# Optimization experiments

Hardware: AMD Instinct MI355X
Metric: run time of the kernel (lower is better)

## Reference

```python
import jax, jax.numpy as jnp
import numpy as np

D_MODEL = 1024
N_HEADS = 16
FF_DIM = 4096
EPS = 1e-05


def setup_inputs() -> dict:
    key = jax.random.key(0)
    ks = jax.random.split(key, 8)
    B, T, E, F = 4, 2048, D_MODEL, FF_DIM
    s = 0.02
    return {
        "encoder_input": jax.random.normal(ks[0], (B, T, E), jnp.float32),
        "source_padding_masks": jax.random.randint(ks[1], (B, T), 0, 2, jnp.int32),
        "Wq": jax.random.normal(ks[2], (E, E), jnp.float32) * s,
        "Wk": jax.random.normal(ks[3], (E, E), jnp.float32) * s,
        "Wv": jax.random.normal(ks[4], (E, E), jnp.float32) * s,
        "Wo": jax.random.normal(ks[5], (E, E), jnp.float32) * s,
        "w1": jax.random.normal(ks[6], (F, E), jnp.float32) * s,
        "b1": jnp.zeros((F,), jnp.float32),
        "w2": jax.random.normal(ks[7], (E, F), jnp.float32) * s,
        "b2": jnp.zeros((E,), jnp.float32),
        "ln_g": jnp.ones((E,), jnp.float32),
        "ln_b": jnp.zeros((E,), jnp.float32),
    }


def _layer_norm(x, g, b):
    # Faithful to the custom LayerNorm: unbiased std (ddof=1), eps added to sd.
    mean = jnp.mean(x, axis=-1, keepdims=True)
    sd = jnp.std(x, axis=-1, keepdims=True, ddof=1)
    return (x - mean) / (sd + EPS) * g + b


def reference(encoder_input, source_padding_masks, Wq, Wk, Wv, Wo, w1, b1, w2, b2, ln_g, ln_b):
    x = encoder_input
    B, T, E = x.shape
    H, hd = N_HEADS, E // N_HEADS

    q = (x @ Wq.T).reshape(B, T, H, hd).transpose(0, 2, 1, 3)  # [B,H,T,hd]
    k = (x @ Wk.T).reshape(B, T, H, hd).transpose(0, 2, 1, 3)
    v = (x @ Wv.T).reshape(B, T, H, hd).transpose(0, 2, 1, 3)

    scores = jnp.einsum("bhqd,bhkd->bhqk", q, k) / jnp.sqrt(jnp.float32(hd))
    key_mask = source_padding_masks[:, None, None, :]  # [B,1,1,T]
    scores = jnp.where(key_mask == 0, -jnp.inf, scores)
    attn = jax.nn.softmax(scores, axis=-1)
    attn = attn * source_padding_masks[:, None, :, None].astype(attn.dtype)  # query mask post-softmax

    ctx = jnp.einsum("bhqk,bhkd->bhqd", attn, v)
    ctx = ctx.transpose(0, 2, 1, 3).reshape(B, T, E)
    att_out = ctx @ Wo.T

    # residual block 1 (dropout is identity in eval)
    h = _layer_norm(att_out + x, ln_g, ln_b)

    ff = jax.nn.relu(h @ w1.T + b1) @ w2.T + b2
    # residual block 2 (same shared LayerNorm params)
    out = _layer_norm(ff + h, ln_g, ln_b)
    return out
```

## Files before the change

### kernel.cpp

```cpp
#include <hip/hip_runtime.h>
#include <hip/hip_bf16.h>


typedef __attribute__((ext_vector_type(8))) short  short8;
typedef __attribute__((ext_vector_type(4))) float  f32x4;
typedef __attribute__((ext_vector_type(4))) int    i32x4;
typedef __attribute__((ext_vector_type(4))) unsigned short u16x4;

__device__ inline float b2f(unsigned short u) {
    unsigned int x = ((unsigned int)u) << 16;
    return __builtin_bit_cast(float, x);
}
__device__ inline unsigned short f2b(float f) {
    return __builtin_bit_cast(unsigned short, __float2bfloat16(f));
}

__device__ inline void llds16(const unsigned short* g, unsigned short* l) {
    __builtin_amdgcn_global_load_lds(
        (const __attribute__((address_space(1))) unsigned int*)g,
        (__attribute__((address_space(3))) unsigned int*)l, 16, 0, 0);
}

__device__ inline int swz(int row, int col8) {
    return (row << 6) + (((col8 ^ (row >> 1)) & 7) << 3);
}

__global__ __launch_bounds__(256)
void cast_f32_bf16(const float* __restrict__ in, unsigned short* __restrict__ out,
                   int n4)
{
    int i = blockIdx.x * 256 + threadIdx.x;
    if (i >= n4) return;
    f32x4 v = *(const f32x4*)(in + (size_t)i * 4);
    u16x4 o;
    for (int j = 0; j < 4; ++j) o[j] = f2b(v[j]);
    *(u16x4*)(out + (size_t)i * 4) = o;
}

__global__ __launch_bounds__(256)
void mask_bf16(const int* __restrict__ m, unsigned short* __restrict__ mb, int n)
{
    int i = blockIdx.x * 256 + threadIdx.x;
    if (i < n) mb[i] = m[i] ? (unsigned short)0x3F80 : (unsigned short)0;
}

template <int BIAS, int RELU, int VT>
__global__ __launch_bounds__(256, 2)
void gemm_bt(const unsigned short* __restrict__ A,
             const unsigned short* __restrict__ W,
             const float* __restrict__ bias,
             const int* __restrict__ mask,
             unsigned short* __restrict__ C,
             int M, int N, int K)
{
    __shared__ __attribute__((aligned(16))) unsigned short a_s[128 * 64];
    __shared__ __attribute__((aligned(16))) unsigned short b_s[128 * 64];

    const int tid  = threadIdx.x;
    const int lane = tid & 63;
    const int w    = tid >> 6;
    const int ln   = lane & 15;
    const int quad = lane >> 4;
    const int wm   = w >> 1, wn = w & 1;
    const int bm   = blockIdx.y, bn = blockIdx.x;

    f32x4 acc[4][4] = {};

    const int nkt = K >> 6;
    for (int kt = 0; kt < nkt; ++kt) {
        for (int i = 0; i < 4; ++i) {
            int e   = i * 256 + tid;
            int row = e >> 3;
            int c8  = (e & 7) ^ ((e >> 4) & 7);
            llds16(A + (size_t)(bm * 128 + row) * K + kt * 64 + c8 * 8, &a_s[e * 8]);
            llds16(W + (size_t)(bn * 128 + row) * K + kt * 64 + c8 * 8, &b_s[e * 8]);
        }
        __syncthreads();
        for (int ks = 0; ks < 2; ++ks) {
            short8 af[4], bf_[4];
            for (int mt = 0; mt < 4; ++mt)
                af[mt] = *(const short8*)&a_s[swz(wm * 64 + mt * 16 + ln, ks * 4 + quad)];
            for (int nt = 0; nt < 4; ++nt)
                bf_[nt] = *(const short8*)&b_s[swz(wn * 64 + nt * 16 + ln, ks * 4 + quad)];
            for (int mt = 0; mt < 4; ++mt)
                for (int nt = 0; nt < 4; ++nt)
                    acc[mt][nt] = __builtin_amdgcn_mfma_f32_16x16x32_bf16(
                        af[mt], bf_[nt], acc[mt][nt], 0, 0, 0);
        }
        __syncthreads();
    }

    if (VT) {
        const int T2 = 2048, H2 = 16;
        for (int mt = 0; mt < 4; ++mt) {
            int row0 = bm * 128 + wm * 64 + mt * 16 + quad * 4;
            int bb = row0 >> 11, t0 = row0 & 2047;
            i32x4 mi = *(const i32x4*)&mask[bb * 2048 + t0];
            for (int nt = 0; nt < 4; ++nt) {
                int col = bn * 128 + wn * 64 + nt * 16 + ln;
                int hh2 = col >> 6, d = col & 63;
                u16x4 o;
                for (int r = 0; r < 4; ++r)
                    o[r] = mi[r] ? f2b(acc[mt][nt][r]) : (unsigned short)0;
                *(u16x4*)(C + ((size_t)((bb * H2 + hh2) * 64 + d)) * T2 + t0) = o;
            }
        }
    } else {
        for (int nt = 0; nt < 4; ++nt) {
            int col = bn * 128 + wn * 64 + nt * 16 + ln;
            float bv = 0.f;
            if (BIAS) bv = bias[col];
            for (int mt = 0; mt < 4; ++mt) {
                int row0 = bm * 128 + wm * 64 + mt * 16 + quad * 4;
                for (int r = 0; r < 4; ++r) {
                    float v = acc[mt][nt][r] + bv;
                    if (RELU) v = v > 0.f ? v : 0.f;
                    C[(size_t)(row0 + r) * N + col] = f2b(v);
                }
            }
        }
    }
}

__global__ __launch_bounds__(256, 4)
void flash_attn3(const unsigned short* __restrict__ Q,
                 const unsigned short* __restrict__ K,
                 const unsigned short* __restrict__ Vt,
                 const unsigned short* __restrict__ mb,
                 const int* __restrict__ mask,
                 unsigned short* __restrict__ O,
                 int T, int H, int E)
{
    __shared__ __attribute__((aligned(16))) unsigned short k_s[2][64 * 64];
    __shared__ __attribute__((aligned(16))) unsigned short v_s[2][64 * 64];
    __shared__ __attribute__((aligned(16))) unsigned short p_s[64 * 64];

    const int qt = blockIdx.x, h = blockIdx.y, b = blockIdx.z;
    const int tid  = threadIdx.x;
    const int w    = tid >> 6;
    const int lane = tid & 63;
    const int ln   = lane & 15;
    const int quad = lane >> 4;
    const int q0   = qt * 64;
    const unsigned short* vt_b = Vt + (size_t)(b * H + h) * 64 * T;

    for (int i = 0; i < 2; ++i) {
        int e = i * 256 + tid;
        int row = e >> 3;
        int c8  = (e & 7) ^ ((e >> 4) & 7);
        llds16(Q + (size_t)(b * T + q0 + row) * E + h * 64 + c8 * 8, &p_s[e * 8]);
        llds16(K + (size_t)(b * T + row) * E + h * 64 + c8 * 8, &k_s[0][e * 8]);
        llds16(vt_b + (size_t)row * T + c8 * 8, &v_s[0][e * 8]);
    }
    __syncthreads();
    short8 aq[2];
    aq[0] = *(const short8*)&p_s[w * 1024 + swz(ln, quad)];
    aq[1] = *(const short8*)&p_s[w * 1024 + swz(ln, 4 + quad)];

    f32x4 Oa[4] = {};
    f32x4 lacc = {};
    const float SCL = 0.125f * 1.44269504f;

    const int nkb = T >> 6;
    for (int kb = 0; kb < nkb; ++kb) {
        const int cur = kb & 1;
        if (kb + 1 < nkb) {
            for (int i = 0; i < 2; ++i) {
                int e = i * 256 + tid;
                int row = e >> 3;
                int c8  = (e & 7) ^ ((e >> 4) & 7);
                llds16(K + (size_t)(b * T + (kb + 1) * 64 + row) * E + h * 64 + c8 * 8,
                       &k_s[cur ^ 1][e * 8]);
                llds16(vt_b + (size_t)row * T + (kb + 1) * 64 + c8 * 8,
                       &v_s[cur ^ 1][e * 8]);
            }
        }
        short8 mf0 = *(const short8*)&mb[b * T + kb * 64 + quad * 8];
        short8 mf1 = *(const short8*)&mb[b * T + kb * 64 + 32 + quad * 8];

        f32x4 S[4] = {};
        for (int ks = 0; ks < 2; ++ks)
            for (int nt = 0; nt < 4; ++nt) {
                short8 bf_ = *(const short8*)&k_s[cur][swz(nt * 16 + ln, ks * 4 + quad)];
                S[nt] = __builtin_amdgcn_mfma_f32_16x16x32_bf16(aq[ks], bf_, S[nt], 0, 0, 0);
            }
        for (int nt = 0; nt < 4; ++nt)
            for (int r = 0; r < 4; ++r) {
                float p = exp2f(S[nt][r] * SCL);
                p_s[w * 1024 + swz(quad * 4 + r, 2 * nt + (ln >> 3)) + (ln & 7)] = f2b(p);
            }
        short8 ap0 = *(const short8*)&p_s[w * 1024 + swz(ln, quad)];
        short8 ap1 = *(const short8*)&p_s[w * 1024 + swz(ln, 4 + quad)];
        lacc = __builtin_amdgcn_mfma_f32_16x16x32_bf16(ap0, mf0, lacc, 0, 0, 0);
        lacc = __builtin_amdgcn_mfma_f32_16x16x32_bf16(ap1, mf1, lacc, 0, 0, 0);
        for (int nt = 0; nt < 4; ++nt) {
            short8 bv0 = *(const short8*)&v_s[cur][swz(nt * 16 + ln, quad)];
            Oa[nt] = __builtin_amdgcn_mfma_f32_16x16x32_bf16(ap0, bv0, Oa[nt], 0, 0, 0);
            short8 bv1 = *(const short8*)&v_s[cur][swz(nt * 16 + ln, 4 + quad)];
            Oa[nt] = __builtin_amdgcn_mfma_f32_16x16x32_bf16(ap1, bv1, Oa[nt], 0, 0, 0);
        }
        __syncthreads();
    }

    for (int r = 0; r < 4; ++r) {
        int qrow = q0 + w * 16 + quad * 4 + r;
        float inv = mask[b * T + qrow] ? 1.f / lacc[r] : 0.f;
        for (int nt = 0; nt < 4; ++nt)
            O[(size_t)(b * T + qrow) * E + h * 64 + nt * 16 + ln] = f2b(Oa[nt][r] * inv);
    }
}

template <int R_F32, int O_F32>
__global__ __launch_bounds__(256, 4)
void ln_residual(const unsigned short* __restrict__ A,
                 const void* __restrict__ R,
                 const float* __restrict__ G,
                 const float* __restrict__ Bt,
                 void* __restrict__ Y, int E)
{
    const int row = blockIdx.x;
    const int tid = threadIdx.x;
    size_t base = (size_t)row * E + tid * 4;
    u16x4 a4 = *(const u16x4*)(A + base);
    float rv[4];
    if (R_F32) {
        f32x4 r4 = *(const f32x4*)((const float*)R + base);
        for (int j = 0; j < 4; ++j) rv[j] = r4[j];
    } else {
        u16x4 r4 = *(const u16x4*)((const unsigned short*)R + base);
        for (int j = 0; j < 4; ++j) rv[j] = b2f(r4[j]);
    }
    float v[4]; float s = 0.f, sq = 0.f;
    for (int j = 0; j < 4; ++j) {
        v[j] = b2f(a4[j]) + rv[j];
        s += v[j]; sq += v[j] * v[j];
    }
    for (int o = 32; o; o >>= 1) {
        s  += __shfl_xor(s, o, 64);
        sq += __shfl_xor(sq, o, 64);
    }
    __shared__ float red[8];
    int w = tid >> 6, lane = tid & 63;
    if (lane == 0) { red[w] = s; red[4 + w] = sq; }
    __syncthreads();
    s  = red[0] + red[1] + red[2] + red[3];
    sq = red[4] + red[5] + red[6] + red[7];
    float mean = s / E;
    float var  = (sq - s * mean) / (E - 1);
    var = fmaxf(var, 0.f);
    float inv = 1.f / (sqrtf(var) + 1e-5f);
    f32x4 g4 = *(const f32x4*)(G + tid * 4);
    f32x4 b4 = *(const f32x4*)(Bt + tid * 4);
    if (O_F32) {
        f32x4 o4;
        for (int j = 0; j < 4; ++j)
            o4[j] = (v[j] - mean) * inv * g4[j] + b4[j];
        *(f32x4*)((float*)Y + base) = o4;
    } else {
        u16x4 o4;
        for (int j = 0; j < 4; ++j)
            o4[j] = f2b((v[j] - mean) * inv * g4[j] + b4[j]);
        *(u16x4*)((unsigned short*)Y + base) = o4;
    }
}

extern "C" void kernel_launch(void* const* d_in, const int* in_sizes, int n_in,
                              void* d_out, int out_size, void* d_ws, size_t ws_size,
                              hipStream_t stream)
{
    const int B = 4, T = 2048, E = 1024, F = 4096, H = 16;
    const int M = B * T;

    const float* x  = (const float*)d_in[0];
    const int* mask = (const int*)d_in[1];
    const float* Wq = (const float*)d_in[2];
    const float* Wk = (const float*)d_in[3];
    const float* Wv = (const float*)d_in[4];
    const float* Wo = (const float*)d_in[5];
    const float* w1 = (const float*)d_in[6];
    const float* b1 = (const float*)d_in[7];
    const float* w2 = (const float*)d_in[8];
    const float* b2 = (const float*)d_in[9];
    const float* lg = (const float*)d_in[10];
    const float* lb = (const float*)d_in[11];
    float* out = (float*)d_out;

    char* ws = (char*)d_ws;
    const size_t MB = 1024 * 1024;
    unsigned short* xb  = (unsigned short*)(ws);
    unsigned short* q   = (unsigned short*)(ws + 16 * MB);
    unsigned short* kk  = (unsigned short*)(ws + 32 * MB);
    unsigned short* vt  = (unsigned short*)(ws + 48 * MB);
    unsigned short* ctx = (unsigned short*)(ws + 64 * MB);
    unsigned short* hh  = (unsigned short*)(ws + 80 * MB);
    unsigned short* mbf = hh;
    unsigned short* ff1 = (unsigned short*)(ws);
    unsigned short* ff2 = ctx;
    unsigned short* att = q;
    unsigned short* Wqb = (unsigned short*)(ws + 96 * MB);
    unsigned short* Wkb = (unsigned short*)(ws + 98 * MB);
    unsigned short* Wvb = (unsigned short*)(ws + 100 * MB);
    unsigned short* Wob = (unsigned short*)(ws + 102 * MB);
    unsigned short* w1b = (unsigned short*)(ws + 104 * MB);
    unsigned short* w2b = (unsigned short*)(ws + 112 * MB);

    dim3 blk(256);
    cast_f32_bf16<<<dim3(M * E / 4 / 256), blk, 0, stream>>>(x,  xb,  M * E / 4);
    cast_f32_bf16<<<dim3(E * E / 4 / 256), blk, 0, stream>>>(Wq, Wqb, E * E / 4);
    cast_f32_bf16<<<dim3(E * E / 4 / 256), blk, 0, stream>>>(Wk, Wkb, E * E / 4);
    cast_f32_bf16<<<dim3(E * E / 4 / 256), blk, 0, stream>>>(Wv, Wvb, E * E / 4);
    cast_f32_bf16<<<dim3(E * E / 4 / 256), blk, 0, stream>>>(Wo, Wob, E * E / 4);
    cast_f32_bf16<<<dim3(F * E / 4 / 256), blk, 0, stream>>>(w1, w1b, F * E / 4);
    cast_f32_bf16<<<dim3(F * E / 4 / 256), blk, 0, stream>>>(w2, w2b, F * E / 4);
    mask_bf16<<<dim3(M / 256), blk, 0, stream>>>(mask, mbf, M);

    gemm_bt<0, 0, 0><<<dim3(E / 128, M / 128), blk, 0, stream>>>(xb, Wqb, nullptr, nullptr, q,  M, E, E);
    gemm_bt<0, 0, 0><<<dim3(E / 128, M / 128), blk, 0, stream>>>(xb, Wkb, nullptr, nullptr, kk, M, E, E);
    gemm_bt<0, 0, 1><<<dim3(E / 128, M / 128), blk, 0, stream>>>(xb, Wvb, nullptr, mask, vt, M, E, E);
    flash_attn3<<<dim3(T / 64, H, B), blk, 0, stream>>>(q, kk, vt, mbf, mask, ctx, T, H, E);
    gemm_bt<0, 0, 0><<<dim3(E / 128, M / 128), blk, 0, stream>>>(ctx, Wob, nullptr, nullptr, att, M, E, E);
    ln_residual<1, 0><<<dim3(M), blk, 0, stream>>>(att, x, lg, lb, hh, E);
    gemm_bt<1, 1, 0><<<dim3(F / 128, M / 128), blk, 0, stream>>>(hh, w1b, b1, nullptr, ff1, M, F, E);
    gemm_bt<1, 0, 0><<<dim3(E / 128, M / 128), blk, 0, stream>>>(ff1, w2b, b2, nullptr, ff2, M, E, F);
    ln_residual<0, 1><<<dim3(M), blk, 0, stream>>>(ff2, hh, lg, lb, out, E);
}
```

Before: 585.3 us.

## Rewrite flash attention with 32x32 MFMA, register-resident P, and prescaled Q

```diff
diff --git a/kernel.cpp b/kernel.cpp
--- a/kernel.cpp
+++ b/kernel.cpp
@@ -2,10 +2,12 @@
 #include <hip/hip_bf16.h>
 
 
-typedef __attribute__((ext_vector_type(8))) short  short8;
-typedef __attribute__((ext_vector_type(4))) float  f32x4;
-typedef __attribute__((ext_vector_type(4))) int    i32x4;
-typedef __attribute__((ext_vector_type(4))) unsigned short u16x4;
+typedef __attribute__((ext_vector_type(8)))  short  short8;
+typedef __attribute__((ext_vector_type(4)))  float  f32x4;
+typedef __attribute__((ext_vector_type(16))) float  f32x16;
+typedef __attribute__((ext_vector_type(4)))  int    i32x4;
+typedef __attribute__((ext_vector_type(4)))  unsigned int   u32x4;
+typedef __attribute__((ext_vector_type(4)))  unsigned short u16x4;
 
 __device__ inline float b2f(unsigned short u) {
     unsigned int x = ((unsigned int)u) << 16;
@@ -38,13 +40,13 @@
 }
 
 __global__ __launch_bounds__(256)
-void mask_bf16(const int* __restrict__ m, unsigned short* __restrict__ mb, int n)
+void mask_f32(const int* __restrict__ m, float* __restrict__ mf, int n)
 {
     int i = blockIdx.x * 256 + threadIdx.x;
-    if (i < n) mb[i] = m[i] ? (unsigned short)0x3F80 : (unsigned short)0;
-}
-
-template <int BIAS, int RELU, int VT>
+    if (i < n) mf[i] = m[i] ? 1.f : 0.f;
+}
+
+template <int BIAS, int RELU, int VT, int SC = 0>
 __global__ __launch_bounds__(256, 2)
 void gemm_bt(const unsigned short* __restrict__ A,
              const unsigned short* __restrict__ W,
@@ -115,6 +117,7 @@
                 for (int r = 0; r < 4; ++r) {
                     float v = acc[mt][nt][r] + bv;
                     if (RELU) v = v > 0.f ? v : 0.f;
+                    if (SC)   v *= 0.18033688f;
                     C[(size_t)(row0 + r) * N + col] = f2b(v);
                 }
             }
@@ -123,43 +126,48 @@
 }
 
 __global__ __launch_bounds__(256, 4)
-void flash_attn3(const unsigned short* __restrict__ Q,
+void flash_attn5(const unsigned short* __restrict__ Q,
                  const unsigned short* __restrict__ K,
                  const unsigned short* __restrict__ Vt,
-                 const unsigned short* __restrict__ mb,
+                 const float* __restrict__ mf,
                  const int* __restrict__ mask,
                  unsigned short* __restrict__ O,
                  int T, int H, int E)
 {
     __shared__ __attribute__((aligned(16))) unsigned short k_s[2][64 * 64];
     __shared__ __attribute__((aligned(16))) unsigned short v_s[2][64 * 64];
-    __shared__ __attribute__((aligned(16))) unsigned short p_s[64 * 64];
-
-    const int qt = blockIdx.x, h = blockIdx.y, b = blockIdx.z;
+
+    const int ord = blockIdx.x;
+    const int wg  = (ord & 7) * 128 + (ord >> 3);
+    const int qt  = wg & 15;
+    const int h   = (wg >> 4) & 15;
+    const int b   = wg >> 8;
+
     const int tid  = threadIdx.x;
     const int w    = tid >> 6;
     const int lane = tid & 63;
-    const int ln   = lane & 15;
-    const int quad = lane >> 4;
-    const int q0   = qt * 64;
+    const int lq   = lane & 31;
+    const int hl   = lane >> 5;
+    const bool hi  = (hl != 0);
+    const int q0   = qt * 128 + w * 32;
     const unsigned short* vt_b = Vt + (size_t)(b * H + h) * 64 * T;
+
+    const unsigned short* qp = Q + (size_t)(b * T + q0 + lq) * E + h * 64 + hl * 8;
+    short8 aq[4];
+#pragma unroll
+    for (int s = 0; s < 4; ++s) aq[s] = *(const short8*)(qp + s * 16);
 
     for (int i = 0; i < 2; ++i) {
         int e = i * 256 + tid;
         int row = e >> 3;
         int c8  = (e & 7) ^ ((e >> 4) & 7);
-        llds16(Q + (size_t)(b * T + q0 + row) * E + h * 64 + c8 * 8, &p_s[e * 8]);
         llds16(K + (size_t)(b * T + row) * E + h * 64 + c8 * 8, &k_s[0][e * 8]);
         llds16(vt_b + (size_t)row * T + c8 * 8, &v_s[0][e * 8]);
     }
     __syncthreads();
-    short8 aq[2];
-    aq[0] = *(const short8*)&p_s[w * 1024 + swz(ln, quad)];
-    aq[1] = *(const short8*)&p_s[w * 1024 + swz(ln, 4 + quad)];
-
-    f32x4 Oa[4] = {};
-    f32x4 lacc = {};
-    const float SCL = 0.125f * 1.44269504f;
+
+    f32x16 Oa0 = {}, Oa1 = {};
+    float lrun = 0.f;
 
     const int nkb = T >> 6;
     for (int kb = 0; kb < nkb; ++kb) {
@@ -175,38 +183,75 @@
                        &v_s[cur ^ 1][e * 8]);
             }
         }
-        short8 mf0 = *(const short8*)&mb[b * T + kb * 64 + quad * 8];
-        short8 mf1 = *(const short8*)&mb[b * T + kb * 64 + 32 + quad * 8];
-
-        f32x4 S[4] = {};
-        for (int ks = 0; ks < 2; ++ks)
-            for (int nt = 0; nt < 4; ++nt) {
-                short8 bf_ = *(const short8*)&k_s[cur][swz(nt * 16 + ln, ks * 4 + quad)];
-                S[nt] = __builtin_amdgcn_mfma_f32_16x16x32_bf16(aq[ks], bf_, S[nt], 0, 0, 0);
-            }
-        for (int nt = 0; nt < 4; ++nt)
-            for (int r = 0; r < 4; ++r) {
-                float p = exp2f(S[nt][r] * SCL);
-                p_s[w * 1024 + swz(quad * 4 + r, 2 * nt + (ln >> 3)) + (ln & 7)] = f2b(p);
-            }
-        short8 ap0 = *(const short8*)&p_s[w * 1024 + swz(ln, quad)];
-        short8 ap1 = *(const short8*)&p_s[w * 1024 + swz(ln, 4 + quad)];
-        lacc = __builtin_amdgcn_mfma_f32_16x16x32_bf16(ap0, mf0, lacc, 0, 0, 0);
-        lacc = __builtin_amdgcn_mfma_f32_16x16x32_bf16(ap1, mf1, lacc, 0, 0, 0);
-        for (int nt = 0; nt < 4; ++nt) {
-            short8 bv0 = *(const short8*)&v_s[cur][swz(nt * 16 + ln, quad)];
-            Oa[nt] = __builtin_amdgcn_mfma_f32_16x16x32_bf16(ap0, bv0, Oa[nt], 0, 0, 0);
-            short8 bv1 = *(const short8*)&v_s[cur][swz(nt * 16 + ln, 4 + quad)];
-            Oa[nt] = __builtin_amdgcn_mfma_f32_16x16x32_bf16(ap1, bv1, Oa[nt], 0, 0, 0);
+
+        f32x16 S0 = {}, S1 = {};
+#pragma unroll
+        for (int s = 0; s < 4; ++s) {
+            short8 kf0 = *(const short8*)&k_s[cur][swz(lq, 2 * s + hl)];
+            S0 = __builtin_amdgcn_mfma_f32_32x32x16_bf16(kf0, aq[s], S0, 0, 0, 0);
+            short8 kf1 = *(const short8*)&k_s[cur][swz(32 + lq, 2 * s + hl)];
+            S1 = __builtin_amdgcn_mfma_f32_32x32x16_bf16(kf1, aq[s], S1, 0, 0, 0);
+        }
+
+        const float* mrow = mf + b * T + kb * 64 + hl * 4;
+        unsigned int c[8][2];
+        float sl = 0.f;
+#pragma unroll
+        for (int g = 0; g < 4; ++g) {
+            f32x4 mv = *(const f32x4*)(mrow + g * 8);
+            float p0 = exp2f(S0[g * 4 + 0]) * mv[0];
+            float p1 = exp2f(S0[g * 4 + 1]) * mv[1];
+            float p2 = exp2f(S0[g * 4 + 2]) * mv[2];
+            float p3 = exp2f(S0[g * 4 + 3]) * mv[3];
+            sl += (p0 + p1) + (p2 + p3);
+            c[g][0] = (unsigned int)f2b(p0) | ((unsigned int)f2b(p1) << 16);
+            c[g][1] = (unsigned int)f2b(p2) | ((unsigned int)f2b(p3) << 16);
+        }
+#pragma unroll
+        for (int g = 0; g < 4; ++g) {
+            f32x4 mv = *(const f32x4*)(mrow + 32 + g * 8);
+            float p0 = exp2f(S1[g * 4 + 0]) * mv[0];
+            float p1 = exp2f(S1[g * 4 + 1]) * mv[1];
+            float p2 = exp2f(S1[g * 4 + 2]) * mv[2];
+            float p3 = exp2f(S1[g * 4 + 3]) * mv[3];
+            sl += (p0 + p1) + (p2 + p3);
+            c[4 + g][0] = (unsigned int)f2b(p0) | ((unsigned int)f2b(p1) << 16);
+            c[4 + g][1] = (unsigned int)f2b(p2) | ((unsigned int)f2b(p3) << 16);
+        }
+        sl += __shfl_xor(sl, 32);
+        lrun += sl;
+
+#pragma unroll
+        for (int kt = 0; kt < 4; ++kt) {
+            unsigned int x0 = c[2 * kt][0],     x1 = c[2 * kt][1];
+            unsigned int y0 = c[2 * kt + 1][0], y1 = c[2 * kt + 1][1];
+            unsigned int xs0 = (unsigned int)__shfl_xor((int)x0, 32);
+            unsigned int xs1 = (unsigned int)__shfl_xor((int)x1, 32);
+            unsigned int ys0 = (unsigned int)__shfl_xor((int)y0, 32);
+            unsigned int ys1 = (unsigned int)__shfl_xor((int)y1, 32);
+            u32x4 wv;
+            wv[0] = hi ? ys0 : x0;
+            wv[1] = hi ? ys1 : x1;
+            wv[2] = hi ? y0 : xs0;
+            wv[3] = hi ? y1 : xs1;
+            short8 pw = __builtin_bit_cast(short8, wv);
+            short8 vf0 = *(const short8*)&v_s[cur][swz(lq, 2 * kt + hl)];
+            Oa0 = __builtin_amdgcn_mfma_f32_32x32x16_bf16(pw, vf0, Oa0, 0, 0, 0);
+            short8 vf1 = *(const short8*)&v_s[cur][swz(32 + lq, 2 * kt + hl)];
+            Oa1 = __builtin_amdgcn_mfma_f32_32x32x16_bf16(pw, vf1, Oa1, 0, 0, 0);
         }
         __syncthreads();
     }
 
-    for (int r = 0; r < 4; ++r) {
-        int qrow = q0 + w * 16 + quad * 4 + r;
-        float inv = mask[b * T + qrow] ? 1.f / lacc[r] : 0.f;
-        for (int nt = 0; nt < 4; ++nt)
-            O[(size_t)(b * T + qrow) * E + h * 64 + nt * 16 + ln] = f2b(Oa[nt][r] * inv);
+    float inv_own = mask[b * T + q0 + lq] ? 1.f / lrun : 0.f;
+    const size_t obase = (size_t)(b * T) * E + (size_t)h * 64;
+#pragma unroll
+    for (int r = 0; r < 16; ++r) {
+        int qrl = (r & 3) + 8 * (r >> 2) + 4 * hl;
+        float inv = __shfl(inv_own, qrl);
+        size_t orow = obase + (size_t)(q0 + qrl) * E;
+        O[orow + lq]      = f2b(Oa0[r] * inv);
+        O[orow + 32 + lq] = f2b(Oa1[r] * inv);
     }
 }
 
@@ -293,7 +338,7 @@
     unsigned short* vt  = (unsigned short*)(ws + 48 * MB);
     unsigned short* ctx = (unsigned short*)(ws + 64 * MB);
     unsigned short* hh  = (unsigned short*)(ws + 80 * MB);
-    unsigned short* mbf = hh;
+    float*          mfb = (float*)(ws + 80 * MB);
     unsigned short* ff1 = (unsigned short*)(ws);
     unsigned short* ff2 = ctx;
     unsigned short* att = q;
@@ -312,12 +357,12 @@
     cast_f32_bf16<<<dim3(E * E / 4 / 256), blk, 0, stream>>>(Wo, Wob, E * E / 4);
     cast_f32_bf16<<<dim3(F * E / 4 / 256), blk, 0, stream>>>(w1, w1b, F * E / 4);
     cast_f32_bf16<<<dim3(F * E / 4 / 256), blk, 0, stream>>>(w2, w2b, F * E / 4);
-    mask_bf16<<<dim3(M / 256), blk, 0, stream>>>(mask, mbf, M);
-
-    gemm_bt<0, 0, 0><<<dim3(E / 128, M / 128), blk, 0, stream>>>(xb, Wqb, nullptr, nullptr, q,  M, E, E);
-    gemm_bt<0, 0, 0><<<dim3(E / 128, M / 128), blk, 0, stream>>>(xb, Wkb, nullptr, nullptr, kk, M, E, E);
-    gemm_bt<0, 0, 1><<<dim3(E / 128, M / 128), blk, 0, stream>>>(xb, Wvb, nullptr, mask, vt, M, E, E);
-    flash_attn3<<<dim3(T / 64, H, B), blk, 0, stream>>>(q, kk, vt, mbf, mask, ctx, T, H, E);
+    mask_f32<<<dim3(M / 256), blk, 0, stream>>>(mask, mfb, M);
+
+    gemm_bt<0, 0, 0, 1><<<dim3(E / 128, M / 128), blk, 0, stream>>>(xb, Wqb, nullptr, nullptr, q,  M, E, E);
+    gemm_bt<0, 0, 0>   <<<dim3(E / 128, M / 128), blk, 0, stream>>>(xb, Wkb, nullptr, nullptr, kk, M, E, E);
+    gemm_bt<0, 0, 1>   <<<dim3(E / 128, M / 128), blk, 0, stream>>>(xb, Wvb, nullptr, mask, vt, M, E, E);
+    flash_attn5<<<dim3((T / 128) * H * B), blk, 0, stream>>>(q, kk, vt, mfb, mask, ctx, T, H, E);
     gemm_bt<0, 0, 0><<<dim3(E / 128, M / 128), blk, 0, stream>>>(ctx, Wob, nullptr, nullptr, att, M, E, E);
     ln_residual<1, 0><<<dim3(M), blk, 0, stream>>>(att, x, lg, lb, hh, E);
     gemm_bt<1, 1, 0><<<dim3(F / 128, M / 128), blk, 0, stream>>>(hh, w1b, b1, nullptr, ff1, M, F, E);
```

Measured after the change: 552.8 us. 5.6% less time.
